# Kernel optimization log

Measured on AMD Instinct MI355X. Metric: run time of the kernel, lower is better.

Reference implementation:

```python
import jax, jax.numpy as jnp
import numpy as np

# Multi-scale deformable attention (MSDeformAttn) with the pytorch grid_sample
# fallback semantics: bilinear, padding_mode='zeros', align_corners=False.
SPATIAL_SHAPES = [(128, 128), (64, 64), (32, 32), (16, 16)]  # (H_l, W_l)
N, C, M, L, P = 2, 256, 8, 4, 4
D = C // M
LEN_IN = sum(h * w for h, w in SPATIAL_SHAPES)  # 21760


def setup_inputs() -> dict:
    key = jax.random.key(0)
    ks = jax.random.split(key, 11)
    s = 0.02
    return {
        "query": jax.random.normal(ks[0], (N, LEN_IN, C), jnp.float32),
        "reference_points": jax.random.uniform(ks[1], (N, LEN_IN, L, 2), jnp.float32),
        "input_flatten": jax.random.normal(ks[2], (N, LEN_IN, C), jnp.float32),
        "W_off": jax.random.normal(ks[3], (C, M * L * P * 2), jnp.float32) * s,
        "b_off": jax.random.normal(ks[4], (M * L * P * 2,), jnp.float32) * s,
        "W_attn": jax.random.normal(ks[5], (C, M * L * P), jnp.float32) * s,
        "b_attn": jax.random.normal(ks[6], (M * L * P,), jnp.float32) * s,
        "W_val": jax.random.normal(ks[7], (C, C), jnp.float32) * s,
        "b_val": jax.random.normal(ks[8], (C,), jnp.float32) * s,
        "W_out": jax.random.normal(ks[9], (C, C), jnp.float32) * s,
        "b_out": jax.random.normal(ks[10], (C,), jnp.float32) * s,
    }


def _bilinear_sample(val_flat, gx, gy, H, W):
    """grid_sample(bilinear, zeros, align_corners=False) on one level.
    val_flat: (N, M, H*W, D); gx, gy: (N, M, Lq*P) in [-1, 1] (any value)."""
    x = (gx + 1.0) * (W * 0.5) - 0.5
    y = (gy + 1.0) * (H * 0.5) - 0.5
    x0 = jnp.floor(x)
    y0 = jnp.floor(y)
    wx1 = x - x0  # fractional parts
    wy1 = y - y0
    x0i = x0.astype(jnp.int32)
    y0i = y0.astype(jnp.int32)

    def gather(ix, iy):
        valid = (ix >= 0) & (ix < W) & (iy >= 0) & (iy < H)
        idx = jnp.clip(iy, 0, H - 1) * W + jnp.clip(ix, 0, W - 1)
        g = jnp.take_along_axis(val_flat, idx[..., None], axis=2)  # (N,M,LqP,D)
        return g * valid[..., None].astype(val_flat.dtype)

    g00 = gather(x0i, y0i)
    g01 = gather(x0i + 1, y0i)
    g10 = gather(x0i, y0i + 1)
    g11 = gather(x0i + 1, y0i + 1)
    return (g00 * ((1 - wx1) * (1 - wy1))[..., None]
            + g01 * (wx1 * (1 - wy1))[..., None]
            + g10 * ((1 - wx1) * wy1)[..., None]
            + g11 * (wx1 * wy1)[..., None])


def reference(query, reference_points, input_flatten, W_off, b_off,
              W_attn, b_attn, W_val, b_val, W_out, b_out):
    Nq, Lq, _ = query.shape
    # value projection -> (N, Len_in, M, D)
    value = (input_flatten @ W_val + b_val).reshape(Nq, -1, M, D)
    # sampling offsets -> (N, Lq, M, L, P, 2)
    offsets = (query @ W_off + b_off).reshape(Nq, Lq, M, L, P, 2)
    # attention weights: softmax over L*P
    attn = jax.nn.softmax((query @ W_attn + b_attn).reshape(Nq, Lq, M, L * P), axis=-1)
    attn = attn.reshape(Nq, Lq, M, L, P)
    # offset normalizer is (W_l, H_l)
    norm = jnp.array([[w, h] for h, w in SPATIAL_SHAPES], jnp.float32)  # (L, 2)
    loc = reference_points[:, :, None, :, None, :] + offsets / norm[None, None, None, :, None, :]
    grid = 2.0 * loc - 1.0  # (N, Lq, M, L, P, 2)

    acc = jnp.zeros((Nq, M, Lq, D), value.dtype)
    start = 0
    for lvl, (H, W) in enumerate(SPATIAL_SHAPES):
        val_flat = value[:, start:start + H * W].transpose(0, 2, 1, 3)  # (N,M,HW,D)
        gx = grid[:, :, :, lvl, :, 0].transpose(0, 2, 1, 3).reshape(Nq, M, Lq * P)
        gy = grid[:, :, :, lvl, :, 1].transpose(0, 2, 1, 3).reshape(Nq, M, Lq * P)
        samp = _bilinear_sample(val_flat, gx, gy, H, W).reshape(Nq, M, Lq, P, D)
        w_l = attn[:, :, :, lvl, :].transpose(0, 2, 1, 3)  # (N, M, Lq, P)
        acc = acc + jnp.einsum('nmqpd,nmqp->nmqd', samp, w_l)
        start += H * W

    out = acc.transpose(0, 2, 1, 3).reshape(Nq, Lq, C)  # (N, Lq, C)
    return out @ W_out + b_out
```

## Files before the change

### kernel.cpp

```cpp
#include <hip/hip_runtime.h>
#include <hip/hip_fp16.h>
#include <math.h>
#include <stdint.h>


constexpr int NB  = 2;
constexpr int C   = 256;
constexpr int M   = 8;
constexpr int D   = 32;
constexpr int LEN = 21760;
constexpr int QCHc = LEN / 2;

typedef __attribute__((ext_vector_type(8))) short short8v;
typedef __attribute__((ext_vector_type(4))) float f32x4;

__device__ __forceinline__ short f2bf(float x) {
  uint32_t u = __float_as_uint(x);
  u = (u + 0x7fffu + ((u >> 16) & 1u)) >> 16;
  return (short)u;
}

__global__ __launch_bounds__(256) void k_wpack(
    const float* __restrict__ Wval, const float* __restrict__ Woff,
    const float* __restrict__ Wattn, const float* __restrict__ Wout,
    short* __restrict__ WvP, short* __restrict__ WdP, short* __restrict__ WoP) {
  const int job = blockIdx.y;
  const int ncols = (job == 1) ? 384 : 256;
  const int NCG = ncols / 16;
  const int elems = 256 * ncols;
  const int idx = blockIdx.x * 256 + threadIdx.x;
  if (idx >= elems) return;
  const int e    = idx & 7;
  const int lane = (idx >> 3) & 63;
  const int lr = lane & 15, lk = lane >> 4;
  const int cgks = idx >> 9;
  const int cg = cgks % NCG, ks = cgks / NCG;
  const int k = ks * 32 + lk * 8 + e;
  const int col = cg * 16 + lr;
  float v;
  if (job == 0)      v = Wval[(size_t)k * 256 + col];
  else if (job == 2) v = Wout[(size_t)k * 256 + col];
  else               v = (col < 256) ? Woff[(size_t)k * 256 + col]
                                     : Wattn[(size_t)k * 128 + col - 256];
  short* dst = (job == 0) ? WvP : (job == 1) ? WdP : WoP;
  dst[idx] = f2bf(v);
}

__device__ __forceinline__ short8v ldBP(const short* __restrict__ WP, int NCG,
                                        int cg, int ks, int lane) {
  const int4 v = *(const int4*)(WP + ((size_t)((ks * NCG + cg) * 64 + lane)) * 8);
  union { int4 i; short8v s; } u; u.i = v; return u.s;
}

__device__ __forceinline__ void stage_cast(const float* __restrict__ p, char* sm, int t) {
  const int r = t >> 3, seg = t & 7;
  const float4* s = (const float4*)(p + (size_t)r * C + seg * 32);
  short v[32];
#pragma unroll
  for (int i = 0; i < 8; ++i) {
    float4 f = s[i];
    v[i * 4 + 0] = f2bf(f.x); v[i * 4 + 1] = f2bf(f.y);
    v[i * 4 + 2] = f2bf(f.z); v[i * 4 + 3] = f2bf(f.w);
  }
#pragma unroll
  for (int i = 0; i < 4; ++i) {
    const int kb = (seg * 32 + i * 8) * 2;
    *(int4*)(sm + r * 512 + (kb ^ ((r & 7) << 4))) = ((const int4*)v)[i];
  }
}

__device__ __forceinline__ void stage_bf16(const short* __restrict__ p, char* sm, int t) {
  const int r = t >> 3, seg = t & 7;
  const int4* s = (const int4*)(p + (size_t)r * C + seg * 32);
#pragma unroll
  for (int i = 0; i < 4; ++i) {
    const int kb = (seg * 32 + i * 8) * 2;
    *(int4*)(sm + r * 512 + (kb ^ ((r & 7) << 4))) = s[i];
  }
}

__device__ __forceinline__ short8v ldsA(const char* sm, int lane, int rt, int ks) {
  const int row = rt * 16 + (lane & 15);
  const int kb  = ks * 64 + ((lane >> 4) << 4);
  const int4 v = *(const int4*)(sm + row * 512 + (kb ^ ((row & 7) << 4)));
  union { int4 i; short8v s; } u; u.i = v; return u.s;
}

#define MFMA __builtin_amdgcn_mfma_f32_16x16x32_bf16

#define GEMM_BODY(WP)                                                       \
  short8v a[2][8];                                                          \
  _Pragma("unroll") for (int rt = 0; rt < 2; ++rt)                          \
  _Pragma("unroll") for (int ks = 0; ks < 8; ++ks)                          \
      a[rt][ks] = ldsA(smA, lane, rt, ks);                                  \
  f32x4 acc[2][4];                                                          \
  _Pragma("unroll") for (int rt = 0; rt < 2; ++rt)                          \
  _Pragma("unroll") for (int ct = 0; ct < 4; ++ct)                          \
      acc[rt][ct] = (f32x4){0.f, 0.f, 0.f, 0.f};                            \
  short8v b0[8], b1[8];                                                     \
  _Pragma("unroll") for (int ks = 0; ks < 8; ++ks)                          \
      b0[ks] = ldBP(WP, 16, cg0 + 0, ks, lane);                             \
  _Pragma("unroll") for (int ks = 0; ks < 8; ++ks)                          \
      b1[ks] = ldBP(WP, 16, cg0 + 1, ks, lane);                             \
  _Pragma("unroll") for (int ks = 0; ks < 8; ++ks) {                        \
    acc[0][0] = MFMA(a[0][ks], b0[ks], acc[0][0], 0, 0, 0);                 \
    acc[1][0] = MFMA(a[1][ks], b0[ks], acc[1][0], 0, 0, 0);                 \
  }                                                                         \
  _Pragma("unroll") for (int ks = 0; ks < 8; ++ks)                          \
      b0[ks] = ldBP(WP, 16, cg0 + 2, ks, lane);                             \
  _Pragma("unroll") for (int ks = 0; ks < 8; ++ks) {                        \
    acc[0][1] = MFMA(a[0][ks], b1[ks], acc[0][1], 0, 0, 0);                 \
    acc[1][1] = MFMA(a[1][ks], b1[ks], acc[1][1], 0, 0, 0);                 \
  }                                                                         \
  _Pragma("unroll") for (int ks = 0; ks < 8; ++ks)                          \
      b1[ks] = ldBP(WP, 16, cg0 + 3, ks, lane);                             \
  _Pragma("unroll") for (int ks = 0; ks < 8; ++ks) {                        \
    acc[0][2] = MFMA(a[0][ks], b0[ks], acc[0][2], 0, 0, 0);                 \
    acc[1][2] = MFMA(a[1][ks], b0[ks], acc[1][2], 0, 0, 0);                 \
  }                                                                         \
  _Pragma("unroll") for (int ks = 0; ks < 8; ++ks) {                        \
    acc[0][3] = MFMA(a[0][ks], b1[ks], acc[0][3], 0, 0, 0);                 \
    acc[1][3] = MFMA(a[1][ks], b1[ks], acc[1][3], 0, 0, 0);                 \
  }

__global__ __launch_bounds__(256, 2) void k_valproj(
    const float* __restrict__ infl, const short* __restrict__ WvP,
    const float* __restrict__ bv, __half* __restrict__ value) {
  __shared__ __align__(16) char smA[16384];
  const int t = threadIdx.x, lane = t & 63, w = t >> 6;
  const int r0 = blockIdx.x * 32;
  stage_cast(infl + (size_t)r0 * C, smA, t);
  __syncthreads();
  const int cg0 = w * 4;
  const int lr = lane & 15, lk = lane >> 4;
  GEMM_BODY(WvP)

  const int n = (blockIdx.x >= (LEN / 32)) ? 1 : 0;
  const int pixbase = r0 - n * LEN;
#pragma unroll
  for (int ct = 0; ct < 4; ++ct) {
    const int col = (cg0 + ct) * 16 + lr;
    const float bb = bv[col];
    const int m = col >> 5, d = col & 31;
    __half* vp = value + ((size_t)(n * 8 + m) * LEN) * 32 + d;
#pragma unroll
    for (int rt = 0; rt < 2; ++rt)
#pragma unroll
      for (int r = 0; r < 4; ++r) {
        const int pix = pixbase + rt * 16 + lk * 4 + r;
        vp[(size_t)pix * 32] = __float2half(acc[rt][ct][r] + bb);
      }
  }
}

__global__ __launch_bounds__(256, 2) void k_outproj(
    const short* __restrict__ accB, const short* __restrict__ WoP,
    const float* __restrict__ bo, float* __restrict__ out) {
  __shared__ __align__(16) char smA[16384];
  const int t = threadIdx.x, lane = t & 63, w = t >> 6;
  const int r0 = blockIdx.x * 32;
  stage_bf16(accB + (size_t)r0 * C, smA, t);
  __syncthreads();
  const int cg0 = w * 4;
  const int lr = lane & 15, lk = lane >> 4;
  GEMM_BODY(WoP)

#pragma unroll
  for (int ct = 0; ct < 4; ++ct) {
    const int col = (cg0 + ct) * 16 + lr;
    const float bb = bo[col];
#pragma unroll
    for (int rt = 0; rt < 2; ++rt)
#pragma unroll
      for (int r = 0; r < 4; ++r) {
        const int row = r0 + rt * 16 + lk * 4 + r;
        out[(size_t)row * C + col] = acc[rt][ct][r] + bb;
      }
  }
}

__global__ __launch_bounds__(256, 3) void k_desc(
    const float* __restrict__ query, const float* __restrict__ refp,
    const short* __restrict__ WdP, const float* __restrict__ boff,
    const float* __restrict__ battn, uint2* __restrict__ descD, int qbase) {
  __shared__ __align__(16) char smem[50176];
  char*  smA  = smem;
  float* offs = (float*)smem;
  float* attw = (float*)(smem + 32768);
  float* refs = (float*)(smem + 49152);

  const int t = threadIdx.x, lane = t & 63, w = t >> 6;
  const int n   = blockIdx.x / 340;
  const int q0c = (blockIdx.x % 340) * 32;
  const size_t qrow = (size_t)n * LEN + qbase + q0c;

  refs[t] = refp[qrow * 8 + t];
  stage_cast(query + qrow * C, smA, t);
  __syncthreads();

  f32x4 acc[2][6];
#pragma unroll
  for (int a = 0; a < 2; ++a)
#pragma unroll
    for (int b = 0; b < 6; ++b) acc[a][b] = (f32x4){0.f, 0.f, 0.f, 0.f};
  const int cgb = w * 6;
#pragma unroll
  for (int ks = 0; ks < 8; ++ks) {
    const short8v a0 = ldsA(smA, lane, 0, ks);
    const short8v a1 = ldsA(smA, lane, 1, ks);
#pragma unroll
    for (int ct = 0; ct < 6; ++ct) {
      const short8v b = ldBP(WdP, 24, cgb + ct, ks, lane);
      acc[0][ct] = MFMA(a0, b, acc[0][ct], 0, 0, 0);
      acc[1][ct] = MFMA(a1, b, acc[1][ct], 0, 0, 0);
    }
  }
  __syncthreads();

#pragma unroll
  for (int ct = 0; ct < 6; ++ct) {
    const int col = (cgb + ct) * 16 + (lane & 15);
    const float bb = (col < 256) ? boff[col] : battn[col - 256];
#pragma unroll
    for (int rt = 0; rt < 2; ++rt)
#pragma unroll
      for (int r = 0; r < 4; ++r) {
        const int row = rt * 16 + ((lane >> 4) << 2) + r;
        const float vv = acc[rt][ct][r] + bb;
        if (col < 256) offs[row * 256 + col] = vv;
        else           attw[row * 128 + col - 256] = vv;
      }
  }
  __syncthreads();

  {
    const int q = t >> 3, m = t & 7;
    float v[16], mx = -1e30f;
#pragma unroll
    for (int j = 0; j < 16; ++j) { v[j] = attw[q * 128 + m * 16 + j]; mx = fmaxf(mx, v[j]); }
    float s = 0.f;
#pragma unroll
    for (int j = 0; j < 16; ++j) { v[j] = __expf(v[j] - mx); s += v[j]; }
    const float inv = 1.f / s;
#pragma unroll
    for (int j = 0; j < 16; ++j) attw[q * 128 + m * 16 + j] = v[j] * inv;
  }
  __syncthreads();

#pragma unroll
  for (int i = 0; i < 16; ++i) {
    const int e = i * 256 + t;
    const int q = e >> 7, rem = e & 127;
    const int m = rem >> 4, j = rem & 15, l = j >> 2;
    const int jo = m * 16 + j;
    const float ox = offs[q * 256 + 2 * jo], oy = offs[q * 256 + 2 * jo + 1];
    const float aw = attw[q * 128 + jo];
    const float rx = refs[q * 8 + l * 2 + 0], ry = refs[q * 8 + l * 2 + 1];
    const int W = 128 >> l;
    const float x = rx * (float)W + ox - 0.5f;
    const float y = ry * (float)W + oy - 0.5f;
    const float xc = fminf(fmaxf(x, -8.f), 503.f);
    const float yc = fminf(fmaxf(y, -8.f), 503.f);
    const uint32_t xfix = (uint32_t)((xc + 8.f) * 128.f + 0.5f);
    const uint32_t yfix = (uint32_t)((yc + 8.f) * 128.f + 0.5f);
    uint2 dsc;
    dsc.x = xfix | (yfix << 16);
    dsc.y = (uint32_t)__half_as_ushort(__float2half_rn(aw));
    descD[((size_t)(n * 8 + m) * QCHc + q0c + q) * 16 + j] = dsc;
  }
}

__global__ __launch_bounds__(256, 3) void k_gather(
    const uint2* __restrict__ descD, const __half* __restrict__ value,
    short* __restrict__ accB, int qbase) {
  const int t = threadIdx.x;
  const int d4 = t & 3, ql = t >> 2;
  const int bid = blockIdx.x;
  const int s = bid & 15, qc = bid >> 4;
  const int n = s >> 3, m = s & 7;
  const int q = qc * 64 + ql;
  const uint4* dp4 = (const uint4*)(descD + ((size_t)(n * 8 + m) * QCHc + q) * 16);
  const char* vb = (const char*)value +
                   (size_t)((n * 8 + m) * LEN) * 64 + d4 * 16;

  uint4 dd[8];
#pragma unroll
  for (int i = 0; i < 8; ++i) dd[i] = dp4[i];
  __builtin_amdgcn_sched_barrier(0);

  float accf[8];
#pragma unroll
  for (int i = 0; i < 8; ++i) accf[i] = 0.f;

  union V { uint4 v; __half2 h[4]; };
  V r0_, r1_, r2_, r3_, r4_, r5_, r6_, r7_;
  V r8_, r9_, rA_, rB_, rC_, rD_, rE_, rF_;
  __half2 hw[4][4];

#define DECJ(J, KK, RA, RB, RC, RD)                                           \
  {                                                                           \
    constexpr int l_ = (J) >> 2;                                              \
    constexpr int W_ = 128 >> l_;                                             \
    constexpr int stl_ = (l_ == 0) ? 0 : (l_ == 1) ? 16384 : (l_ == 2) ? 20480 : 21504; \
    const uint32_t lo_ = ((J) & 1) ? dd[(J) >> 1].z : dd[(J) >> 1].x;         \
    const uint32_t hi_ = ((J) & 1) ? dd[(J) >> 1].w : dd[(J) >> 1].y;         \
    const int xf_ = (int)(lo_ & 0xffffu), yf_ = (int)(lo_ >> 16);             \
    const float aw_ = __half2float(__ushort_as_half((unsigned short)(hi_ & 0xffffu))); \
    const int xi_ = (xf_ >> 7) - 8, yi_ = (yf_ >> 7) - 8;                     \
    const float fx_ = (float)(xf_ & 127) * 0.0078125f;                        \
    const float fy_ = (float)(yf_ & 127) * 0.0078125f;                        \
    float wx0_ = 1.f - fx_, wx1_ = fx_, wy0_ = 1.f - fy_, wy1_ = fy_;         \
    if (xi_ < 0 || xi_ >= W_)         wx0_ = 0.f;                             \
    if (xi_ + 1 < 0 || xi_ + 1 >= W_) wx1_ = 0.f;                             \
    if (yi_ < 0 || yi_ >= W_)         wy0_ = 0.f;                             \
    if (yi_ + 1 < 0 || yi_ + 1 >= W_) wy1_ = 0.f;                             \
    const int x0_ = min(max(xi_, 0), W_ - 1), x1_ = min(max(xi_ + 1, 0), W_ - 1); \
    const int y0_ = min(max(yi_, 0), W_ - 1), y1_ = min(max(yi_ + 1, 0), W_ - 1); \
    hw[KK][0] = __float2half2_rn(wx0_ * wy0_ * aw_);                          \
    hw[KK][1] = __float2half2_rn(wx1_ * wy0_ * aw_);                          \
    hw[KK][2] = __float2half2_rn(wx0_ * wy1_ * aw_);                          \
    hw[KK][3] = __float2half2_rn(wx1_ * wy1_ * aw_);                          \
    RA.v = *(const uint4*)(vb + (size_t)(stl_ + y0_ * W_ + x0_) * 64u);       \
    RB.v = *(const uint4*)(vb + (size_t)(stl_ + y0_ * W_ + x1_) * 64u);       \
    RC.v = *(const uint4*)(vb + (size_t)(stl_ + y1_ * W_ + x0_) * 64u);       \
    RD.v = *(const uint4*)(vb + (size_t)(stl_ + y1_ * W_ + x1_) * 64u);       \
  }

#define CONSJ(KK, RA, RB, RC, RD, ACH)                                        \
  {                                                                           \
    _Pragma("unroll") for (int i_ = 0; i_ < 4; ++i_) {                        \
      ACH[i_] = __hfma2(RA.h[i_], hw[KK][0], ACH[i_]);                        \
      ACH[i_] = __hfma2(RB.h[i_], hw[KK][1], ACH[i_]);                        \
      ACH[i_] = __hfma2(RC.h[i_], hw[KK][2], ACH[i_]);                        \
      ACH[i_] = __hfma2(RD.h[i_], hw[KK][3], ACH[i_]);                        \
    }                                                                         \
  }

#define PROM(ACH)                                                             \
  {                                                                           \
    _Pragma("unroll") for (int i_ = 0; i_ < 4; ++i_) {                        \
      const float2 f_ = __half22float2(ACH[i_]);                              \
      accf[2 * i_] += f_.x; accf[2 * i_ + 1] += f_.y;                         \
      ACH[i_] = __float2half2_rn(0.f);                                        \
    }                                                                         \
  }

#define GROUP(G)                                                              \
  {                                                                           \
    DECJ(4 * (G) + 0, 0, r0_, r1_, r2_, r3_)                                  \
    DECJ(4 * (G) + 1, 1, r4_, r5_, r6_, r7_)                                  \
    DECJ(4 * (G) + 2, 2, r8_, r9_, rA_, rB_)                                  \
    DECJ(4 * (G) + 3, 3, rC_, rD_, rE_, rF_)                                  \
    __builtin_amdgcn_sched_barrier(0);                                        \
    __half2 acch[4];                                                          \
    _Pragma("unroll") for (int i_ = 0; i_ < 4; ++i_)                          \
        acch[i_] = __float2half2_rn(0.f);                                     \
    CONSJ(0, r0_, r1_, r2_, r3_, acch)                                        \
    CONSJ(1, r4_, r5_, r6_, r7_, acch)                                        \
    PROM(acch)                                                                \
    CONSJ(2, r8_, r9_, rA_, rB_, acch)                                        \
    CONSJ(3, rC_, rD_, rE_, rF_, acch)                                        \
    PROM(acch)                                                                \
  }

  GROUP(0)
  GROUP(1)
  GROUP(2)
  GROUP(3)
#undef DECJ
#undef CONSJ
#undef PROM
#undef GROUP

  short8v o;
#pragma unroll
  for (int i = 0; i < 8; ++i) o[i] = f2bf(accf[i]);
  *(short8v*)(accB + ((size_t)n * LEN + qbase + q) * 256 + m * 32 + d4 * 8) = o;
}

extern "C" void kernel_launch(void* const* d_in, const int* in_sizes, int n_in,
                              void* d_out, int out_size, void* d_ws, size_t ws_size,
                              hipStream_t stream) {
  const float* query = (const float*)d_in[0];
  const float* refp  = (const float*)d_in[1];
  const float* infl  = (const float*)d_in[2];
  const float* Woff  = (const float*)d_in[3];
  const float* boff  = (const float*)d_in[4];
  const float* Wattn = (const float*)d_in[5];
  const float* battn = (const float*)d_in[6];
  const float* Wval  = (const float*)d_in[7];
  const float* bval  = (const float*)d_in[8];
  const float* Wout  = (const float*)d_in[9];
  const float* bout  = (const float*)d_in[10];
  float* out = (float*)d_out;

  char* ws = (char*)d_ws;
  __half* value = (__half*)ws;
  short*  accB  = (short*)(ws + 22282240);
  uint2*  desc8 = (uint2*)(ws + 44564480);
  short*  WvP   = (short*)(ws + 66846720);
  short*  WdP   = (short*)(ws + 66977792);
  short*  WoP   = (short*)(ws + 67174400);

  k_wpack<<<dim3(384, 3), 256, 0, stream>>>(Wval, Woff, Wattn, Wout,
                                            WvP, WdP, WoP);

  k_valproj<<<(NB * LEN) / 32, 256, 0, stream>>>(infl, WvP, bval, value);

  for (int c = 0; c < 2; ++c) {
    k_desc<<<NB * (QCHc / 32), 256, 0, stream>>>(query, refp, WdP, boff, battn,
                                                 desc8, c * QCHc);
    k_gather<<<16 * (QCHc / 64), 256, 0, stream>>>(desc8, value, accB, c * QCHc);
  }

  k_outproj<<<(NB * LEN) / 32, 256, 0, stream>>>(accB, WoP, bout, out);
}
```

Measured before the change: 153.2 us.

## Double-buffer bilinear gathers across point pairs to overlap loads with FMAs

The sampling kernel now splits its 16 sampling points into 8 groups of two and alternates two register buffers, issuing the gathers for the next group before consuming the previous one. Before, all loads for a group of four points were issued and then fully consumed before the next group started. The aim is to keep memory loads in flight while half-precision FMAs run, hiding gather latency. Live registers stay about the same (two buffers of 8 vectors versus 16 before), but the fp16 partial sum now spans two points between promotions to fp32 instead of two per promotion, which shifts accumulation order slightly.

```diff
diff --git a/kernel.cpp b/kernel.cpp
--- a/kernel.cpp
+++ b/kernel.cpp
@@ -293,17 +293,16 @@
   for (int i = 0; i < 8; ++i) accf[i] = 0.f;
 
   union V { uint4 v; __half2 h[4]; };
-  V r0_, r1_, r2_, r3_, r4_, r5_, r6_, r7_;
-  V r8_, r9_, rA_, rB_, rC_, rD_, rE_, rF_;
-  __half2 hw[4][4];
-
-#define DECJ(J, KK, RA, RB, RC, RD)                                           \
+  V rA[8], rB[8];
+  __half2 hwA[8], hwB[8];
+
+#define DECJ(G, ODD, R, HW, BASE)                                             \
   {                                                                           \
-    constexpr int l_ = (J) >> 2;                                              \
+    constexpr int l_ = (G) >> 1;                                              \
     constexpr int W_ = 128 >> l_;                                             \
     constexpr int stl_ = (l_ == 0) ? 0 : (l_ == 1) ? 16384 : (l_ == 2) ? 20480 : 21504; \
-    const uint32_t lo_ = ((J) & 1) ? dd[(J) >> 1].z : dd[(J) >> 1].x;         \
-    const uint32_t hi_ = ((J) & 1) ? dd[(J) >> 1].w : dd[(J) >> 1].y;         \
+    const uint32_t lo_ = (ODD) ? dd[G].z : dd[G].x;                           \
+    const uint32_t hi_ = (ODD) ? dd[G].w : dd[G].y;                           \
     const int xf_ = (int)(lo_ & 0xffffu), yf_ = (int)(lo_ >> 16);             \
     const float aw_ = __half2float(__ushort_as_half((unsigned short)(hi_ & 0xffffu))); \
     const int xi_ = (xf_ >> 7) - 8, yi_ = (yf_ >> 7) - 8;                     \
@@ -316,61 +315,55 @@
     if (yi_ + 1 < 0 || yi_ + 1 >= W_) wy1_ = 0.f;                             \
     const int x0_ = min(max(xi_, 0), W_ - 1), x1_ = min(max(xi_ + 1, 0), W_ - 1); \
     const int y0_ = min(max(yi_, 0), W_ - 1), y1_ = min(max(yi_ + 1, 0), W_ - 1); \
-    hw[KK][0] = __float2half2_rn(wx0_ * wy0_ * aw_);                          \
-    hw[KK][1] = __float2half2_rn(wx1_ * wy0_ * aw_);                          \
-    hw[KK][2] = __float2half2_rn(wx0_ * wy1_ * aw_);                          \
-    hw[KK][3] = __float2half2_rn(wx1_ * wy1_ * aw_);                          \
-    RA.v = *(const uint4*)(vb + (size_t)(stl_ + y0_ * W_ + x0_) * 64u);       \
-    RB.v = *(const uint4*)(vb + (size_t)(stl_ + y0_ * W_ + x1_) * 64u);       \
-    RC.v = *(const uint4*)(vb + (size_t)(stl_ + y1_ * W_ + x0_) * 64u);       \
-    RD.v = *(const uint4*)(vb + (size_t)(stl_ + y1_ * W_ + x1_) * 64u);       \
-  }
-
-#define CONSJ(KK, RA, RB, RC, RD, ACH)                                        \
+    HW[(BASE) + 0] = __float2half2_rn(wx0_ * wy0_ * aw_);                     \
+    HW[(BASE) + 1] = __float2half2_rn(wx1_ * wy0_ * aw_);                     \
+    HW[(BASE) + 2] = __float2half2_rn(wx0_ * wy1_ * aw_);                     \
+    HW[(BASE) + 3] = __float2half2_rn(wx1_ * wy1_ * aw_);                     \
+    R[(BASE) + 0].v = *(const uint4*)(vb + (size_t)(stl_ + y0_ * W_ + x0_) * 64u); \
+    R[(BASE) + 1].v = *(const uint4*)(vb + (size_t)(stl_ + y0_ * W_ + x1_) * 64u); \
+    R[(BASE) + 2].v = *(const uint4*)(vb + (size_t)(stl_ + y1_ * W_ + x0_) * 64u); \
+    R[(BASE) + 3].v = *(const uint4*)(vb + (size_t)(stl_ + y1_ * W_ + x1_) * 64u); \
+  }
+
+#define DECG(G, R, HW)                                                        \
+  DECJ(G, 0, R, HW, 0)                                                        \
+  DECJ(G, 1, R, HW, 4)                                                        \
+  __builtin_amdgcn_sched_barrier(0);
+
+#define CONSG(R, HW)                                                          \
   {                                                                           \
-    _Pragma("unroll") for (int i_ = 0; i_ < 4; ++i_) {                        \
-      ACH[i_] = __hfma2(RA.h[i_], hw[KK][0], ACH[i_]);                        \
-      ACH[i_] = __hfma2(RB.h[i_], hw[KK][1], ACH[i_]);                        \
-      ACH[i_] = __hfma2(RC.h[i_], hw[KK][2], ACH[i_]);                        \
-      ACH[i_] = __hfma2(RD.h[i_], hw[KK][3], ACH[i_]);                        \
-    }                                                                         \
-  }
-
-#define PROM(ACH)                                                             \
-  {                                                                           \
-    _Pragma("unroll") for (int i_ = 0; i_ < 4; ++i_) {                        \
-      const float2 f_ = __half22float2(ACH[i_]);                              \
-      accf[2 * i_] += f_.x; accf[2 * i_ + 1] += f_.y;                         \
-      ACH[i_] = __float2half2_rn(0.f);                                        \
-    }                                                                         \
-  }
-
-#define GROUP(G)                                                              \
-  {                                                                           \
-    DECJ(4 * (G) + 0, 0, r0_, r1_, r2_, r3_)                                  \
-    DECJ(4 * (G) + 1, 1, r4_, r5_, r6_, r7_)                                  \
-    DECJ(4 * (G) + 2, 2, r8_, r9_, rA_, rB_)                                  \
-    DECJ(4 * (G) + 3, 3, rC_, rD_, rE_, rF_)                                  \
-    __builtin_amdgcn_sched_barrier(0);                                        \
     __half2 acch[4];                                                          \
     _Pragma("unroll") for (int i_ = 0; i_ < 4; ++i_)                          \
         acch[i_] = __float2half2_rn(0.f);                                     \
-    CONSJ(0, r0_, r1_, r2_, r3_, acch)                                        \
-    CONSJ(1, r4_, r5_, r6_, r7_, acch)                                        \
-    PROM(acch)                                                                \
-    CONSJ(2, r8_, r9_, rA_, rB_, acch)                                        \
-    CONSJ(3, rC_, rD_, rE_, rF_, acch)                                        \
-    PROM(acch)                                                                \
-  }
-
-  GROUP(0)
-  GROUP(1)
-  GROUP(2)
-  GROUP(3)
+    _Pragma("unroll") for (int c_ = 0; c_ < 8; ++c_) {                        \
+      _Pragma("unroll") for (int i_ = 0; i_ < 4; ++i_)                        \
+          acch[i_] = __hfma2(R[c_].h[i_], HW[c_], acch[i_]);                  \
+    }                                                                         \
+    _Pragma("unroll") for (int i_ = 0; i_ < 4; ++i_) {                        \
+      const float2 f_ = __half22float2(acch[i_]);                             \
+      accf[2 * i_] += f_.x; accf[2 * i_ + 1] += f_.y;                         \
+    }                                                                         \
+  }
+
+  DECG(0, rA, hwA)
+  DECG(1, rB, hwB)
+  CONSG(rA, hwA)
+  DECG(2, rA, hwA)
+  CONSG(rB, hwB)
+  DECG(3, rB, hwB)
+  CONSG(rA, hwA)
+  DECG(4, rA, hwA)
+  CONSG(rB, hwB)
+  DECG(5, rB, hwB)
+  CONSG(rA, hwA)
+  DECG(6, rA, hwA)
+  CONSG(rB, hwB)
+  DECG(7, rB, hwB)
+  CONSG(rA, hwA)
+  CONSG(rB, hwB)
 #undef DECJ
-#undef CONSJ
-#undef PROM
-#undef GROUP
+#undef DECG
+#undef CONSG
 
   short8v o;
 #pragma unroll
```

After: 155.9 us. Within noise of the previous version (+1.8%).
